# Kernel tuning notes

Measured on AMD Instinct MI355X. Metric: run time of the kernel, lower is better.

Reference implementation:

```python
import jax, jax.numpy as jnp
import numpy as np

N_EMBED = 8192
EMBED_DIM = 32
BETA = 0.25
EPS_NORM = 1e-12   # torch F.normalize eps
EPS_ENT = 1e-4     # get_entropy eps


def _l2norm(x):
    n = jnp.linalg.norm(x, axis=-1, keepdims=True)
    return x / jnp.maximum(n, EPS_NORM)


def setup_inputs() -> dict:
    key = jax.random.key(0)
    k1, k2 = jax.random.split(key)
    z = jax.random.normal(k1, (32, EMBED_DIM, 32, 32), dtype=jnp.float32)
    # embedding.weight.data.uniform_(-1/n_embed, 1/n_embed)
    embedding = jax.random.uniform(k2, (N_EMBED, EMBED_DIM), dtype=jnp.float32,
                                   minval=-1.0 / N_EMBED, maxval=1.0 / N_EMBED)
    return {"z": z, "embedding": embedding}


def reference(z, embedding):
    batch = z.shape[0]
    # bchw -> bhwc
    zt = jnp.transpose(z, (0, 2, 3, 1))
    # l2_norm branch: cosine distance via negative inner product
    zn = _l2norm(zt)
    z_flat = zn.reshape(-1, EMBED_DIM)            # [N, D], N = B*H*W
    ew = _l2norm(embedding)                       # [K, D]
    d = -jnp.matmul(z_flat, ew.T)                 # [N, K] distance matrix
    idx = jnp.argmin(jax.lax.stop_gradient(d), axis=1)  # [N]
    # codebook usage histogram + entropy
    cb_usage = jax.ops.segment_sum(jnp.ones_like(idx, dtype=jnp.float32), idx,
                                   num_segments=N_EMBED)
    probs = (cb_usage + EPS_ENT) / jnp.sum(cb_usage + EPS_ENT)
    cb_entropy = -jnp.sum(probs * jnp.log(probs))
    # gather + re-normalize (faithful to embedding lookup then F.normalize)
    z_q = _l2norm(embedding[idx]).reshape(zn.shape)
    sg = jax.lax.stop_gradient
    loss = (BETA * jnp.mean(jnp.sum((sg(z_q) - zn) ** 2, axis=-1))
            + jnp.mean(jnp.sum((z_q - sg(zn)) ** 2, axis=-1)))
    # straight-through estimator
    z_q_st = zn + sg(z_q - zn)
    z_q_out = jnp.transpose(z_q_st, (0, 3, 1, 2))  # bhwc -> bchw
    return z_q_out, loss, cb_entropy, idx.reshape(batch, -1)
```

## Files before the change

kernel.cpp:

```cpp
#include <hip/hip_runtime.h>
#include <math.h>

#define N_EMBED 8192
#define DIM 32
#define NQ 32768

#define QPB 512
#define NQG (NQ / QPB)
#define KSPL 8
#define KCHUNK (N_EMBED / KSPL)
#define TILE 128
#define NTILES (KCHUNK / TILE)
#define NPLANE 8
#define LSTRIDE 130

#define LOSS_OFF  1048576
#define ENT_OFF   1048577
#define IDX_OFF   1048578

typedef __attribute__((ext_vector_type(8))) _Float16 half8;
typedef __attribute__((ext_vector_type(4))) float floatx4;

__global__ __launch_bounds__(512, 4) void score_kernel(const float* __restrict__ z,
                                                       const float* __restrict__ e,
                                                       unsigned long long* __restrict__ keys16,
                                                       unsigned* __restrict__ usage,
                                                       float* __restrict__ loss_acc) {
    __shared__ half8 lds[2][NPLANE * LSTRIDE];

    const int t = threadIdx.x;

    if (blockIdx.x == 0) {
        for (int i = t; i < N_EMBED; i += 512)
            __hip_atomic_store(&usage[i], 0u, __ATOMIC_RELAXED, __HIP_MEMORY_SCOPE_AGENT);
        if (t == 0)
            __hip_atomic_store(loss_acc, 0.f, __ATOMIC_RELAXED, __HIP_MEMORY_SCOPE_AGENT);
    }

    const int lane = t & 63;
    const int w = t >> 6;
    const int quad = lane >> 4;
    const int lc = lane & 15;
    const int qg = blockIdx.x & (NQG - 1);
    const int kc = blockIdx.x >> 6;
    const int kbase = kc * KCHUNK;
    const int qbase = qg * QPB + w * 64;

    const int ci = t >> 2;
    const int part = t & 3;

    half8 ah4[4], ah[4], am[4];
#pragma unroll
    for (int qt = 0; qt < 4; ++qt) {
        int q = qbase + qt * 16 + lc;
        const float* zp = z + (q >> 10) * (DIM * 1024) + (q & 1023);
        float x[8];
        float ss = 0.f;
#pragma unroll
        for (int j = 0; j < 8; ++j) {
            x[j] = zp[(quad * 8 + j) * 1024];
            ss = fmaf(x[j], x[j], ss);
        }
        ss += __shfl_xor(ss, 16, 64);
        ss += __shfl_xor(ss, 32, 64);
        float inv = 1.f / fmaxf(sqrtf(ss), 1e-12f);
#pragma unroll
        for (int j = 0; j < 8; ++j) {
            float xx = x[j] * inv;
            _Float16 h = (_Float16)xx;
            _Float16 m = (_Float16)((xx - (float)h) * 4096.0f);
            ah[qt][j] = h;
            ah4[qt][j] = (_Float16)((float)h * 4096.0f);
            am[qt][j] = m;
        }
    }

    auto stage_load = [&](int kt, float (&x)[8]) {
        const int code = kbase + kt * TILE + ci;
        const float4* er = (const float4*)(e + code * DIM) + part * 2;
        float4 v0 = er[0], v1 = er[1];
        x[0] = v0.x; x[1] = v0.y; x[2] = v0.z; x[3] = v0.w;
        x[4] = v1.x; x[5] = v1.y; x[6] = v1.z; x[7] = v1.w;
    };
    auto stage_write = [&](int bsel, float (&x)[8]) {
        float ss = 0.f;
#pragma unroll
        for (int j = 0; j < 8; ++j) ss = fmaf(x[j], x[j], ss);
        ss += __shfl_xor(ss, 1, 64);
        ss += __shfl_xor(ss, 2, 64);
        float inv = 1.f / fmaxf(sqrtf(ss), 1e-12f);
        half8 h8, m8;
#pragma unroll
        for (int j = 0; j < 8; ++j) {
            float xx = x[j] * inv;
            _Float16 h = (_Float16)xx;
            _Float16 m = (_Float16)((xx - (float)h) * 4096.0f);
            h8[j] = h; m8[j] = m;
        }
        lds[bsel][part * LSTRIDE + ci] = h8;
        lds[bsel][(4 + part) * LSTRIDE + ci] = m8;
    };

    float best[16];
    int bk[16];
#pragma unroll
    for (int i = 0; i < 16; ++i) { best[i] = -9000.0f; bk[i] = 0; }

    const floatx4 z4 = {0.f, 0.f, 0.f, 0.f};

    {
        float x0[8];
        stage_load(0, x0);
        stage_write(0, x0);
    }
    __syncthreads();

    for (int kt = 0; kt < NTILES; ++kt) {
        float nx[8];
        if (kt + 1 < NTILES) stage_load(kt + 1, nx);

        const half8* __restrict__ buf = lds[kt & 1];
#pragma unroll 2
        for (int ct = 0; ct < TILE / 16; ++ct) {
            half8 bh = buf[(0 * 4 + quad) * LSTRIDE + ct * 16 + lc];
            half8 bm = buf[(1 * 4 + quad) * LSTRIDE + ct * 16 + lc];
            const int kk = kbase + kt * TILE + ct * 16 + lc;
#pragma unroll
            for (int qt = 0; qt < 4; ++qt) {
                floatx4 acc = __builtin_amdgcn_mfma_f32_16x16x32_f16(ah4[qt], bh, z4, 0, 0, 0);
                acc = __builtin_amdgcn_mfma_f32_16x16x32_f16(ah[qt], bm, acc, 0, 0, 0);
                acc = __builtin_amdgcn_mfma_f32_16x16x32_f16(am[qt], bh, acc, 0, 0, 0);
#pragma unroll
                for (int r = 0; r < 4; ++r) {
                    float d = acc[r];
                    if (d > best[qt * 4 + r]) { best[qt * 4 + r] = d; bk[qt * 4 + r] = kk; }
                }
            }
        }

        if (kt + 1 < NTILES) stage_write((kt + 1) & 1, nx);
        __syncthreads();
    }

#pragma unroll
    for (int i = 0; i < 16; ++i) {
        unsigned ub = __float_as_uint(best[i]);
        ub = (ub & 0x80000000u) ? ~ub : (ub | 0x80000000u);
        unsigned long long key = ((unsigned long long)ub << 32) | (unsigned)(~bk[i]);
#pragma unroll
        for (int msk = 1; msk <= 8; msk <<= 1) {
            unsigned long long o = __shfl_xor(key, msk, 64);
            key = (o > key) ? o : key;
        }
        if (lc == 0) {
            int qt = i >> 2, r = i & 3;
            int q = qbase + qt * 16 + quad * 4 + r;
            __hip_atomic_store(&keys16[kc * NQ + q], key,
                               __ATOMIC_RELAXED, __HIP_MEMORY_SCOPE_AGENT);
        }
    }
}

__global__ __launch_bounds__(128) void finalize_kernel(const float* __restrict__ z,
                                                       const float* __restrict__ e,
                                                       const unsigned long long* __restrict__ keys16,
                                                       unsigned* __restrict__ usage,
                                                       float* __restrict__ loss_acc,
                                                       float* __restrict__ out) {
    int n = blockIdx.x * 128 + threadIdx.x;
    int b  = n >> 10;
    int hw = n & 1023;
    const float* zb = z + b * (DIM * 1024) + hw;

    float q[DIM];
    float ss = 0.f;
#pragma unroll
    for (int d = 0; d < DIM; ++d) {
        q[d] = zb[d * 1024];
        ss = fmaf(q[d], q[d], ss);
    }
    float inv = 1.f / fmaxf(sqrtf(ss), 1e-12f);
#pragma unroll
    for (int d = 0; d < DIM; ++d) q[d] *= inv;

    unsigned long long bestkey = 0ull;
#pragma unroll
    for (int c = 0; c < KSPL; ++c) {
        unsigned long long k16 = __hip_atomic_load(&keys16[c * NQ + n],
                                                   __ATOMIC_RELAXED,
                                                   __HIP_MEMORY_SCOPE_AGENT);
        bestkey = (k16 > bestkey) ? k16 : bestkey;
    }
    int idx = (int)(~(unsigned)(bestkey & 0xFFFFFFFFull));

    atomicAdd(&usage[idx], 1u);

    float wv[DIM];
    float ss2 = 0.f;
    const float4* er = (const float4*)(e + idx * DIM);
#pragma unroll
    for (int d8 = 0; d8 < 8; ++d8) {
        float4 t4 = er[d8];
        wv[d8*4+0] = t4.x; wv[d8*4+1] = t4.y; wv[d8*4+2] = t4.z; wv[d8*4+3] = t4.w;
        ss2 += t4.x*t4.x + t4.y*t4.y + t4.z*t4.z + t4.w*t4.w;
    }
    float inv2 = 1.f / fmaxf(sqrtf(ss2), 1e-12f);

    float lsum = 0.f;
    float* outb = out + b * (DIM * 1024) + hw;
#pragma unroll
    for (int d = 0; d < DIM; ++d) {
        float zq = wv[d] * inv2;
        float diff = zq - q[d];
        lsum = fmaf(diff, diff, lsum);
        outb[d * 1024] = q[d] + (zq - q[d]);
    }
    out[IDX_OFF + n] = (float)idx;

#pragma unroll
    for (int off = 32; off > 0; off >>= 1)
        lsum += __shfl_down(lsum, off, 64);
    __shared__ float wsum[2];
    if ((threadIdx.x & 63) == 0) wsum[threadIdx.x >> 6] = lsum;
    __syncthreads();
    if (threadIdx.x == 0)
        atomicAdd(loss_acc, wsum[0] + wsum[1]);
}

__global__ __launch_bounds__(256) void scalar_kernel(const unsigned* __restrict__ usage,
                                                     const float* __restrict__ loss_acc,
                                                     float* __restrict__ out) {
    __shared__ double sm[256];
    int t = threadIdx.x;
    double local = 0.0;
    const float denom = 32768.8192f;
    for (int k = t; k < N_EMBED; k += 256) {
        unsigned c = __hip_atomic_load(&usage[k], __ATOMIC_RELAXED,
                                       __HIP_MEMORY_SCOPE_AGENT);
        float p = ((float)c + 1e-4f) / denom;
        local += (double)(-(p * logf(p)));
    }
    sm[t] = local;
    __syncthreads();
    for (int s = 128; s > 0; s >>= 1) {
        if (t < s) sm[t] += sm[t + s];
        __syncthreads();
    }
    if (t == 0) {
        float la = __hip_atomic_load(loss_acc, __ATOMIC_RELAXED,
                                     __HIP_MEMORY_SCOPE_AGENT);
        out[LOSS_OFF] = (float)(1.25 * (double)la / 32768.0);
        out[ENT_OFF]  = (float)sm[0];
    }
}

extern "C" void kernel_launch(void* const* d_in, const int* in_sizes, int n_in,
                              void* d_out, int out_size, void* d_ws, size_t ws_size,
                              hipStream_t stream) {
    const float* z   = (const float*)d_in[0];
    const float* emb = (const float*)d_in[1];
    float* out = (float*)d_out;

    char* ws = (char*)d_ws;
    unsigned long long* keys16 = (unsigned long long*)ws;
    unsigned* usage            = (unsigned*)(ws + (2 << 20));
    float* loss_acc            = (float*)(ws + (2 << 20) + 32768);

    score_kernel<<<NQG * KSPL, 512, 0, stream>>>(z, emb, keys16, usage, loss_acc);
    finalize_kernel<<<NQ / 128, 128, 0, stream>>>(z, emb, keys16, usage,
                                                  loss_acc, out);
    scalar_kernel<<<1, 256, 0, stream>>>(usage, loss_acc, out);
}
```

Measured before the change: 130.8 us.

## Precompute split-fp16 codebook in prep kernel and DMA tiles directly to LDS

```diff
diff --git a/kernel.cpp b/kernel.cpp
--- a/kernel.cpp
+++ b/kernel.cpp
@@ -21,22 +21,52 @@
 typedef __attribute__((ext_vector_type(8))) _Float16 half8;
 typedef __attribute__((ext_vector_type(4))) float floatx4;
 
-__global__ __launch_bounds__(512, 4) void score_kernel(const float* __restrict__ z,
-                                                       const float* __restrict__ e,
-                                                       unsigned long long* __restrict__ keys16,
-                                                       unsigned* __restrict__ usage,
-                                                       float* __restrict__ loss_acc) {
-    __shared__ half8 lds[2][NPLANE * LSTRIDE];
-
+__global__ __launch_bounds__(256) void prep_kernel(const float* __restrict__ e,
+                                                   half8* __restrict__ prep,
+                                                   unsigned* __restrict__ usage,
+                                                   float* __restrict__ loss_acc) {
     const int t = threadIdx.x;
-
     if (blockIdx.x == 0) {
-        for (int i = t; i < N_EMBED; i += 512)
+        for (int i = t; i < N_EMBED; i += 256)
             __hip_atomic_store(&usage[i], 0u, __ATOMIC_RELAXED, __HIP_MEMORY_SCOPE_AGENT);
         if (t == 0)
             __hip_atomic_store(loss_acc, 0.f, __ATOMIC_RELAXED, __HIP_MEMORY_SCOPE_AGENT);
     }
 
+    const int g = blockIdx.x * 256 + t;
+    const int code = g >> 2;
+    const int part = g & 3;
+
+    const float4* er = (const float4*)(e + code * DIM) + part * 2;
+    float4 v0 = er[0], v1 = er[1];
+    float x[8] = {v0.x, v0.y, v0.z, v0.w, v1.x, v1.y, v1.z, v1.w};
+    float ss = 0.f;
+#pragma unroll
+    for (int j = 0; j < 8; ++j) ss = fmaf(x[j], x[j], ss);
+    ss += __shfl_xor(ss, 1, 64);
+    ss += __shfl_xor(ss, 2, 64);
+    float inv = 1.f / fmaxf(sqrtf(ss), 1e-12f);
+    half8 h8, m8;
+#pragma unroll
+    for (int j = 0; j < 8; ++j) {
+        float xx = x[j] * inv;
+        _Float16 h = (_Float16)xx;
+        _Float16 m = (_Float16)((xx - (float)h) * 4096.0f);
+        h8[j] = h; m8[j] = m;
+    }
+    const int kc = code >> 10, cc = code & 1023;
+    const int kt = cc >> 7,   ci = cc & 127;
+    const int pb = (kc * NTILES + kt) * NPLANE;
+    prep[(pb + part) * 128 + ci]     = h8;
+    prep[(pb + 4 + part) * 128 + ci] = m8;
+}
+
+__global__ __launch_bounds__(512, 4) void score_kernel(const float* __restrict__ z,
+                                                       const half8* __restrict__ prep,
+                                                       unsigned long long* __restrict__ keys16) {
+    __shared__ half8 lds[2][NPLANE * LSTRIDE];
+
+    const int t = threadIdx.x;
     const int lane = t & 63;
     const int w = t >> 6;
     const int quad = lane >> 4;
@@ -46,9 +76,6 @@
     const int kbase = kc * KCHUNK;
     const int qbase = qg * QPB + w * 64;
 
-    const int ci = t >> 2;
-    const int part = t & 3;
-
     half8 ah4[4], ah[4], am[4];
 #pragma unroll
     for (int qt = 0; qt < 4; ++qt) {
@@ -75,30 +102,17 @@
         }
     }
 
-    auto stage_load = [&](int kt, float (&x)[8]) {
-        const int code = kbase + kt * TILE + ci;
-        const float4* er = (const float4*)(e + code * DIM) + part * 2;
-        float4 v0 = er[0], v1 = er[1];
-        x[0] = v0.x; x[1] = v0.y; x[2] = v0.z; x[3] = v0.w;
-        x[4] = v1.x; x[5] = v1.y; x[6] = v1.z; x[7] = v1.w;
-    };
-    auto stage_write = [&](int bsel, float (&x)[8]) {
-        float ss = 0.f;
-#pragma unroll
-        for (int j = 0; j < 8; ++j) ss = fmaf(x[j], x[j], ss);
-        ss += __shfl_xor(ss, 1, 64);
-        ss += __shfl_xor(ss, 2, 64);
-        float inv = 1.f / fmaxf(sqrtf(ss), 1e-12f);
-        half8 h8, m8;
-#pragma unroll
-        for (int j = 0; j < 8; ++j) {
-            float xx = x[j] * inv;
-            _Float16 h = (_Float16)xx;
-            _Float16 m = (_Float16)((xx - (float)h) * 4096.0f);
-            h8[j] = h; m8[j] = m;
-        }
-        lds[bsel][part * LSTRIDE + ci] = h8;
-        lds[bsel][(4 + part) * LSTRIDE + ci] = m8;
+    const char* prepb = (const char*)prep;
+    auto stage_dma = [&](int bsel, int kt) {
+        const char* gsrc = prepb + ((size_t)((kc * NTILES + kt) * NPLANE + w)) * 2048
+                                 + (size_t)lane * 16;
+        char* lbase = (char*)&lds[bsel][w * LSTRIDE];
+        __builtin_amdgcn_global_load_lds(
+            (const __attribute__((address_space(1))) void*)(gsrc),
+            (__attribute__((address_space(3))) void*)(lbase), 16, 0, 0);
+        __builtin_amdgcn_global_load_lds(
+            (const __attribute__((address_space(1))) void*)(gsrc + 1024),
+            (__attribute__((address_space(3))) void*)(lbase + 1024), 16, 0, 0);
     };
 
     float best[16];
@@ -108,16 +122,11 @@
 
     const floatx4 z4 = {0.f, 0.f, 0.f, 0.f};
 
-    {
-        float x0[8];
-        stage_load(0, x0);
-        stage_write(0, x0);
-    }
+    stage_dma(0, 0);
     __syncthreads();
 
     for (int kt = 0; kt < NTILES; ++kt) {
-        float nx[8];
-        if (kt + 1 < NTILES) stage_load(kt + 1, nx);
+        if (kt + 1 < NTILES) stage_dma((kt + 1) & 1, kt + 1);
 
         const half8* __restrict__ buf = lds[kt & 1];
 #pragma unroll 2
@@ -137,8 +146,6 @@
                 }
             }
         }
-
-        if (kt + 1 < NTILES) stage_write((kt + 1) & 1, nx);
         __syncthreads();
     }
 
@@ -263,10 +270,12 @@
 
     char* ws = (char*)d_ws;
     unsigned long long* keys16 = (unsigned long long*)ws;
-    unsigned* usage            = (unsigned*)(ws + (2 << 20));
-    float* loss_acc            = (float*)(ws + (2 << 20) + 32768);
-
-    score_kernel<<<NQG * KSPL, 512, 0, stream>>>(z, emb, keys16, usage, loss_acc);
+    half8* prep                = (half8*)(ws + (2 << 20));
+    unsigned* usage            = (unsigned*)(ws + (3 << 20));
+    float* loss_acc            = (float*)(ws + (3 << 20) + 32768);
+
+    prep_kernel<<<(N_EMBED * 4) / 256, 256, 0, stream>>>(emb, prep, usage, loss_acc);
+    score_kernel<<<NQG * KSPL, 512, 0, stream>>>(z, prep, keys16);
     finalize_kernel<<<NQ / 128, 128, 0, stream>>>(z, emb, keys16, usage,
                                                   loss_acc, out);
     scalar_kernel<<<1, 256, 0, stream>>>(usage, loss_acc, out);
```

New measurement: 129.3 us. No clear change (-1.2%).
